# Optimization experiments

Measured on AMD Instinct MI355X. Metric: run time of the kernel, lower is better.

Reference implementation:

```python
import jax, jax.numpy as jnp
import numpy as np

K_MSG = 1024   # message length k (rows of G)
N_CODE = 2048  # codeword length n (cols of G)
B = 32768      # number of message blocks


def setup_inputs() -> dict:
    key = jax.random.key(0)
    kb, kg = jax.random.split(key)
    b = jax.random.randint(kb, (B, K_MSG), 0, 2, dtype=jnp.int32)
    G = jax.random.randint(kg, (K_MSG, N_CODE), 0, 2, dtype=jnp.int32)
    return {"b": b, "G": G}


def reference(b, G):
    # GF(2) linear block encode: c = (b @ G) mod 2
    # b: [num_blocks, k] bits (0/1), G: [k, n] generator matrix (0/1)
    b2 = b.astype(jnp.int32)
    G2 = G.astype(jnp.int32)
    c = jnp.mod(jnp.matmul(b2, G2), 2)  # [num_blocks, n]
    return c.astype(jnp.int32)
```

## Files before the change

### kernel.cpp

```cpp
#include <hip/hip_runtime.h>
#include <stdint.h>

typedef unsigned long long u64;
typedef unsigned int u32;
typedef u32 v8u __attribute__((ext_vector_type(8)));

#define K_MSG   1024
#define N_CODE  2048
#define NB      32768
#define KW      16
#define ROWS_TILE 256
#define COLS_TILE 64

__global__ void pack_b_kernel(const int* __restrict__ b, u64* __restrict__ bp,
                              int nwords) {
    const int lane  = threadIdx.x & 63;
    const int wave  = blockIdx.x * (blockDim.x >> 6) + (threadIdx.x >> 6);
    const int nwave = gridDim.x * (blockDim.x >> 6);
    for (int word = wave; word < nwords; word += nwave) {
        int v = b[(size_t)word * 64 + lane];
        u64 m = __ballot((v & 1) != 0);
        if (lane == 0) bp[word] = m;
    }
}

__global__ void pack_g_kernel(const int* __restrict__ G, u64* __restrict__ gp) {
    const int lane = threadIdx.x & 63;
    const int wave = blockIdx.x * (blockDim.x >> 6) + (threadIdx.x >> 6);
    const int w    = wave >> 5;
    const int jb   = wave & 31;
    const int j    = jb * 64 + lane;
    u64 word = 0;
#pragma unroll 16
    for (int t = 0; t < 64; ++t) {
        int v = G[(size_t)(w * 64 + t) * N_CODE + j];
        word |= (u64)(v & 1) << t;
    }
    gp[(size_t)w * N_CODE + j] = word;
}


struct RowRegs { v8u a, b, c, d; };

#define SLOAD_ROW(dst, addr)                                            \
    asm volatile("s_load_dwordx8 %0, %4, 0x0\n\t"                       \
                 "s_load_dwordx8 %1, %4, 0x20\n\t"                      \
                 "s_load_dwordx8 %2, %4, 0x40\n\t"                      \
                 "s_load_dwordx8 %3, %4, 0x60"                          \
                 : "=&s"(dst.a), "=&s"(dst.b), "=&s"(dst.c), "=&s"(dst.d) \
                 : "s"(addr))

#define SWAIT() do { asm volatile("s_waitcnt lgkmcnt(0)" ::: "memory");  \
                     __builtin_amdgcn_sched_barrier(0); } while (0)

#define COMPUTE_STORE(cur, s_) do {                                     \
    u32 a0 = 0, a1 = 0, a2 = 0, a3 = 0;                                 \
    _Pragma("unroll")                                                   \
    for (int i = 0; i < 8; ++i) {                                       \
        a0 ^= cur.a[i] & gl[i];                                         \
        a1 ^= cur.b[i] & gl[8 + i];                                     \
        a2 ^= cur.c[i] & gl[16 + i];                                    \
        a3 ^= cur.d[i] & gl[24 + i];                                    \
    }                                                                   \
    u32 acc = (a0 ^ a1) ^ (a2 ^ a3);                                    \
    op[(size_t)(s_) * 4 * N_CODE] = (int)(__popc(acc) & 1);             \
} while (0)

__global__ __launch_bounds__(256) void encode_main(const u64* __restrict__ bp,
                                                   const u64* __restrict__ gp,
                                                   int* __restrict__ out) {
    const int lane = threadIdx.x & 63;
    const int ty   = threadIdx.x >> 6;
    const int j    = blockIdx.x * COLS_TILE + lane;
    const int r0   = blockIdx.y * ROWS_TILE;

    u32 gl[32];
#pragma unroll
    for (int w = 0; w < KW; ++w) {
        u64 v = gp[(size_t)w * N_CODE + j];
        gl[2 * w]     = (u32)v;
        gl[2 * w + 1] = (u32)(v >> 32);
    }

    const int row_u = __builtin_amdgcn_readfirstlane(r0 + ty);
    const u64* rp = bp + ((size_t)row_u << 4);
    int* __restrict__ op = out + (size_t)(r0 + ty) * N_CODE + j;

    RowRegs A, B;
    SLOAD_ROW(A, rp);
    SWAIT();

#pragma unroll 1
    for (int s = 0; s < 62; s += 2) {
        SLOAD_ROW(B, rp + (size_t)(s + 1) * 64);
        COMPUTE_STORE(A, s);
        SWAIT();
        SLOAD_ROW(A, rp + (size_t)(s + 2) * 64);
        COMPUTE_STORE(B, s + 1);
        SWAIT();
    }
    SLOAD_ROW(B, rp + (size_t)63 * 64);
    COMPUTE_STORE(A, 62);
    SWAIT();
    COMPUTE_STORE(B, 63);
}

__global__ void encode_naive(const int* __restrict__ b, const int* __restrict__ G,
                             int* __restrict__ out) {
    size_t idx = (size_t)blockIdx.x * blockDim.x + threadIdx.x;
    size_t total = (size_t)NB * N_CODE;
    if (idx >= total) return;
    int i = (int)(idx / N_CODE);
    int j = (int)(idx % N_CODE);
    int acc = 0;
    for (int k = 0; k < K_MSG; ++k)
        acc ^= b[(size_t)i * K_MSG + k] & G[(size_t)k * N_CODE + j];
    out[idx] = acc & 1;
}

extern "C" void kernel_launch(void* const* d_in, const int* in_sizes, int n_in,
                              void* d_out, int out_size, void* d_ws, size_t ws_size,
                              hipStream_t stream) {
    const int* b = (const int*)d_in[0];
    const int* G = (const int*)d_in[1];
    int* out = (int*)d_out;

    const size_t bp_bytes = (size_t)NB * KW * sizeof(u64);
    const size_t gp_bytes = (size_t)N_CODE * KW * sizeof(u64);

    if (ws_size < bp_bytes + gp_bytes) {
        size_t total = (size_t)NB * N_CODE;
        encode_naive<<<(unsigned)((total + 255) / 256), 256, 0, stream>>>(b, G, out);
        return;
    }

    u64* bp = (u64*)d_ws;
    u64* gp = (u64*)((char*)d_ws + bp_bytes);

    pack_b_kernel<<<2048, 256, 0, stream>>>(b, bp, NB * KW);
    pack_g_kernel<<<128, 256, 0, stream>>>(G, gp);

    dim3 grid(N_CODE / COLS_TILE, NB / ROWS_TILE);
    encode_main<<<grid, 256, 0, stream>>>(bp, gp, out);
}
```

Before: 157.5 us.

## Compute four output columns per thread with vectorized G loads and stores

```diff
diff --git a/kernel.cpp b/kernel.cpp
--- a/kernel.cpp
+++ b/kernel.cpp
@@ -4,13 +4,15 @@
 typedef unsigned long long u64;
 typedef unsigned int u32;
 typedef u32 v8u __attribute__((ext_vector_type(8)));
+typedef u32 v4u __attribute__((ext_vector_type(4)));
+typedef int v4i __attribute__((ext_vector_type(4)));
 
 #define K_MSG   1024
 #define N_CODE  2048
 #define NB      32768
 #define KW      16
 #define ROWS_TILE 256
-#define COLS_TILE 64
+#define COLS_TILE 256
 
 __global__ void pack_b_kernel(const int* __restrict__ b, u64* __restrict__ bp,
                               int nwords) {
@@ -54,37 +56,45 @@
                      __builtin_amdgcn_sched_barrier(0); } while (0)
 
 #define COMPUTE_STORE(cur, s_) do {                                     \
-    u32 a0 = 0, a1 = 0, a2 = 0, a3 = 0;                                 \
+    v4i r;                                                              \
     _Pragma("unroll")                                                   \
-    for (int i = 0; i < 8; ++i) {                                       \
-        a0 ^= cur.a[i] & gl[i];                                         \
-        a1 ^= cur.b[i] & gl[8 + i];                                     \
-        a2 ^= cur.c[i] & gl[16 + i];                                    \
-        a3 ^= cur.d[i] & gl[24 + i];                                    \
+    for (int c = 0; c < 4; ++c) {                                       \
+        u32 x0 = 0, x1 = 0, x2 = 0, x3 = 0;                             \
+        _Pragma("unroll")                                               \
+        for (int i = 0; i < 8; ++i) {                                   \
+            x0 ^= cur.a[i] & g[c][i];                                   \
+            x1 ^= cur.b[i] & g[c][8 + i];                                \
+            x2 ^= cur.c[i] & g[c][16 + i];                               \
+            x3 ^= cur.d[i] & g[c][24 + i];                               \
+        }                                                               \
+        u32 acc = (x0 ^ x1) ^ (x2 ^ x3);                                \
+        r[c] = (int)(__popc(acc) & 1);                                  \
     }                                                                   \
-    u32 acc = (a0 ^ a1) ^ (a2 ^ a3);                                    \
-    op[(size_t)(s_) * 4 * N_CODE] = (int)(__popc(acc) & 1);             \
+    *(v4i*)(op + (size_t)(s_) * 4 * N_CODE) = r;                        \
 } while (0)
 
-__global__ __launch_bounds__(256) void encode_main(const u64* __restrict__ bp,
-                                                   const u64* __restrict__ gp,
-                                                   int* __restrict__ out) {
+__global__ __launch_bounds__(256, 3) void encode_main(const u64* __restrict__ bp,
+                                                      const u64* __restrict__ gp,
+                                                      int* __restrict__ out) {
     const int lane = threadIdx.x & 63;
     const int ty   = threadIdx.x >> 6;
-    const int j    = blockIdx.x * COLS_TILE + lane;
+    const int j0   = blockIdx.x * COLS_TILE + lane * 4;
     const int r0   = blockIdx.y * ROWS_TILE;
 
-    u32 gl[32];
+    u32 g[4][32];
 #pragma unroll
     for (int w = 0; w < KW; ++w) {
-        u64 v = gp[(size_t)w * N_CODE + j];
-        gl[2 * w]     = (u32)v;
-        gl[2 * w + 1] = (u32)(v >> 32);
+        v4u q0 = *(const v4u*)(gp + (size_t)w * N_CODE + j0);
+        v4u q1 = *(const v4u*)(gp + (size_t)w * N_CODE + j0 + 2);
+        g[0][2 * w] = q0.x; g[0][2 * w + 1] = q0.y;
+        g[1][2 * w] = q0.z; g[1][2 * w + 1] = q0.w;
+        g[2][2 * w] = q1.x; g[2][2 * w + 1] = q1.y;
+        g[3][2 * w] = q1.z; g[3][2 * w + 1] = q1.w;
     }
 
     const int row_u = __builtin_amdgcn_readfirstlane(r0 + ty);
     const u64* rp = bp + ((size_t)row_u << 4);
-    int* __restrict__ op = out + (size_t)(r0 + ty) * N_CODE + j;
+    int* __restrict__ op = out + (size_t)(r0 + ty) * N_CODE + j0;
 
     RowRegs A, B;
     SLOAD_ROW(A, rp);
```

After: 167.5 us. 1.06x slower.
